# Performance work log

Hardware: AMD Instinct MI355X
Metric: run time of the kernel (lower is better)

Reference implementation:

```python
import jax, jax.numpy as jnp
import numpy as np

N_NODES = 50000


def setup_inputs() -> dict:
    key = jax.random.key(0)
    ks = jax.random.split(key, 10)
    B, N, D, H, O = 2, N_NODES, 128, 128, 10
    x = jax.random.normal(ks[0], (B, N, D), dtype=jnp.float32)
    edge_index = jax.random.randint(ks[1], (2, 800000), 0, N, dtype=jnp.int32)
    s = lambda fan_in: 1.0 / np.sqrt(fan_in)
    W  = jax.random.uniform(ks[2], (D, H), jnp.float32, -s(D), s(D))
    b  = jnp.zeros((H,), jnp.float32)
    W1 = jax.random.uniform(ks[3], (H, H // 2), jnp.float32, -s(H), s(H))
    b1 = jnp.zeros((H // 2,), jnp.float32)
    W2 = jax.random.uniform(ks[4], (H // 2, H // 4), jnp.float32, -s(H // 2), s(H // 2))
    b2 = jnp.zeros((H // 4,), jnp.float32)
    W3 = jax.random.uniform(ks[5], (H // 4, O), jnp.float32, -s(H // 4), s(H // 4))
    b3 = jnp.zeros((O,), jnp.float32)
    return {"x": x, "edge_index": edge_index, "W": W, "b": b,
            "W1": W1, "b1": b1, "W2": W2, "b2": b2, "W3": W3, "b3": b3}


def reference(x, edge_index, W, b, W1, b1, W2, b2, W3, b3):
    # GraphConvolution (Kipf): support = x @ W; out[dst] += support[src]; + b
    src, dst = edge_index[0], edge_index[1]
    support = jnp.einsum("bnd,dh->bnh", x, W)          # [B, N, H]
    msgs = support[:, src, :]                            # [B, E, H] gather
    agg = jnp.zeros_like(support).at[:, dst, :].add(msgs)  # scatter-add
    h = jax.nn.gelu(agg + b, approximate=False)          # GELU (torch default erf)
    # dropout is identity at inference (training=False)
    h = jax.nn.relu(jnp.einsum("bnh,hk->bnk", h, W1) + b1)
    h = jax.nn.relu(jnp.einsum("bnk,km->bnm", h, W2) + b2)
    h = jnp.einsum("bnm,mo->bno", h, W3) + b3            # [B, N, O]
    return h.mean(axis=1)                                # [B, O]
```

## Files before the change

### kernel.cpp

```cpp
#include <hip/hip_runtime.h>
#include <math.h>

#define NN 50000
#define DD 128
#define HH 128
#define L1 64
#define L2 32
#define OO 10

#define NW0 16384
#define NW1 8192
#define NW2 2048
#define NWT (NW0 + NW1 + NW2)

typedef short v8s __attribute__((ext_vector_type(8)));
typedef float v4f __attribute__((ext_vector_type(4)));

__device__ __forceinline__ float bf2f_lo(unsigned u) { return __uint_as_float(u << 16); }
__device__ __forceinline__ float bf2f_hi(unsigned u) { return __uint_as_float(u & 0xffff0000u); }
__device__ __forceinline__ unsigned short f2bf(float f) {
    unsigned u = __float_as_uint(f);
    return (unsigned short)((u + 0x7fffu + ((u >> 16) & 1u)) >> 16);
}
__device__ __forceinline__ unsigned pack2(float lo, float hi) {
    return (unsigned)f2bf(lo) | ((unsigned)f2bf(hi) << 16);
}
__device__ __forceinline__ float gelu_f(float v) {
    return 0.5f * v * (1.f + erff(v * 0.70710678118654752f));
}

__global__ __launch_bounds__(256) void k_prep(
    const float* __restrict__ x, unsigned short* __restrict__ xb,
    const int* __restrict__ ei, int* __restrict__ counts,
    const float* __restrict__ W, const float* __restrict__ W1,
    const float* __restrict__ W2, unsigned short* __restrict__ wtp,
    unsigned short* __restrict__ w1tp, unsigned short* __restrict__ w2tp,
    int* __restrict__ ssf, int nfill, unsigned* __restrict__ zrow, int E)
{
    const int gid = blockIdx.x * 256 + threadIdx.x;
    const int stride = gridDim.x * 256;

    for (int i = gid; i < NWT; i += stride) {
        if (i < NW0) {
            const int e = i & 7, ln = (i >> 3) & 63, ks = (i >> 9) & 3, ct = i >> 11;
            wtp[i] = f2bf(W[(ks * 32 + (ln >> 4) * 8 + e) * HH + ct * 16 + (ln & 15)]);
        } else if (i < NW0 + NW1) {
            const int j = i - NW0;
            const int e = j & 7, ln = (j >> 3) & 63, ks = (j >> 9) & 3, ct = j >> 11;
            w1tp[j] = f2bf(W1[(ks * 32 + (ln >> 4) * 8 + e) * L1 + ct * 16 + (ln & 15)]);
        } else {
            const int j = i - NW0 - NW1;
            const int e = j & 7, ln = (j >> 3) & 63, ks = (j >> 9) & 1, ct = j >> 10;
            w2tp[j] = f2bf(W2[(ks * 32 + (ln >> 4) * 8 + e) * L2 + ct * 16 + (ln & 15)]);
        }
    }
    if (zrow != nullptr && gid < 128) zrow[gid] = 0u;
    for (int i = gid; i < nfill; i += stride) ssf[i] = NN;
    const int HALF = NN * 32;
    for (int idx = gid; idx < 2 * HALF; idx += stride) {
        const int b = (idx >= HALF) ? 1 : 0;
        const int j = idx - b * HALF;
        const int n = j >> 5;
        const int c4 = j & 31;
        const float4 v = *(const float4*)(x + ((size_t)b * NN + n) * DD + c4 * 4);
        ushort4 o;
        o.x = f2bf(v.x); o.y = f2bf(v.y); o.z = f2bf(v.z); o.w = f2bf(v.w);
        *(ushort4*)(xb + ((size_t)n * 2 + b) * DD + c4 * 4) = o;
    }
    for (int e = gid; e < E; e += stride)
        atomicAdd(&counts[ei[(size_t)E + e]], 1);
}

__global__ __launch_bounds__(1024) void k_scan1(
    const int* __restrict__ counts, int* __restrict__ offsets,
    int* __restrict__ blksum, int n)
{
    __shared__ int wsum[16], woff[16];
    const int tid = threadIdx.x, lane = tid & 63, wv = tid >> 6;
    const int i = blockIdx.x * 1024 + tid;
    int v = (i < n) ? ((counts[i] + 7) & ~7) : 0;
    int x = v;
    #pragma unroll
    for (int d = 1; d < 64; d <<= 1) { int t = __shfl_up(x, d); if (lane >= d) x += t; }
    if (lane == 63) wsum[wv] = x;
    __syncthreads();
    if (wv == 0 && lane < 16) {
        int y = wsum[lane];
        #pragma unroll
        for (int d = 1; d < 16; d <<= 1) { int t = __shfl_up(y, d); if (lane >= d) y += t; }
        woff[lane] = y - wsum[lane];
        if (lane == 15) blksum[blockIdx.x] = y;
    }
    __syncthreads();
    if (i < n) offsets[i] = woff[wv] + (x - v);
}

__global__ __launch_bounds__(1024) void k_scan2(
    int* __restrict__ offsets, const int* __restrict__ blksum, int nblk, int n)
{
    __shared__ int base_sh, tot_sh;
    const int tid = threadIdx.x, lane = tid & 63, wv = tid >> 6;
    if (wv == 0) {
        int v = (lane < nblk) ? blksum[lane] : 0;
        int x = v;
        #pragma unroll
        for (int d = 1; d < 64; d <<= 1) { int t = __shfl_up(x, d); if (lane >= d) x += t; }
        int incl = __shfl(x, blockIdx.x);
        int own  = __shfl(v, blockIdx.x);
        int tot  = __shfl(x, nblk - 1);
        if (lane == 0) { base_sh = incl - own; tot_sh = tot; }
    }
    __syncthreads();
    const int i = blockIdx.x * 1024 + tid;
    if (i < n) offsets[i] += base_sh;
    if (blockIdx.x == nblk - 1 && tid == 0) offsets[n] = tot_sh;
}

__global__ __launch_bounds__(256) void k_bucket(
    const int* __restrict__ ei, const int* __restrict__ offsets,
    int* __restrict__ cursor, int* __restrict__ ss, int E)
{
    int e = blockIdx.x * 256 + threadIdx.x;
    if (e < E) {
        int d = ei[E + e];
        int pos = offsets[d] + atomicAdd(&cursor[d], 1);
        ss[pos] = ei[e];
    }
}

template<bool FUSED>
__global__ __launch_bounds__(256, 8) void k_mlp_t(
    const unsigned short* __restrict__ src,
    const int* __restrict__ offsets, const int* __restrict__ ss,
    const unsigned short* __restrict__ wtp, const float* __restrict__ b0v,
    const unsigned short* __restrict__ w1tp, const float* __restrict__ b1v,
    const unsigned short* __restrict__ w2tp, const float* __restrict__ b2v,
    float* __restrict__ partials, int srows)
{
    __shared__ __align__(16) unsigned char upool[32 * 136 * 2];
    __shared__ __align__(16) unsigned short h1b[32 * 72];
    __shared__ float b0s[DD], b1s[L1], b2s[L2];
    __shared__ float oacc[64];
    unsigned short* xa  = (unsigned short*)upool;
    unsigned short* hsb = (unsigned short*)upool;
    float* h2p = (float*)upool;

    const int tid = threadIdx.x;
    const int row0 = blockIdx.x * 32;
    const int lane = tid & 63;
    const int w = tid >> 6;

    if (tid < DD) b0s[tid] = b0v[tid];
    if (tid < L1) b1s[tid] = b1v[tid];
    if (tid < L2) b2s[tid] = b2v[tid];
    if (tid < 64) oacc[tid] = 0.f;

    if (FUSED) {
        const int half4 = (lane >> 5) * 4;
        const int co = (lane & 31) * 8;
        #pragma unroll
        for (int j = 0; j < 4; ++j) {
            const int ln = w * 4 + j;
            const int d = blockIdx.x * 16 + ln;
            int s0 = 0, s1 = 0;
            if (d < NN) { s0 = offsets[d]; s1 = offsets[d + 1]; }
            float a[8];
            #pragma unroll
            for (int t = 0; t < 8; ++t) a[t] = 0.f;
            uint4 nidx;
            if (s0 < s1) nidx = *(const uint4*)(ss + s0 + half4);
            for (int i = s0; i < s1; ) {
                const uint4 idx = nidx;
                const int inext = i + 8;
                if (inext < s1) nidx = *(const uint4*)(ss + inext + half4);
                const uint4 r0 = *(const uint4*)(src + (size_t)idx.x * 256 + co);
                const uint4 r1 = *(const uint4*)(src + (size_t)idx.y * 256 + co);
                const uint4 r2 = *(const uint4*)(src + (size_t)idx.z * 256 + co);
                const uint4 r3 = *(const uint4*)(src + (size_t)idx.w * 256 + co);
                a[0] += bf2f_lo(r0.x); a[1] += bf2f_hi(r0.x);
                a[2] += bf2f_lo(r0.y); a[3] += bf2f_hi(r0.y);
                a[4] += bf2f_lo(r0.z); a[5] += bf2f_hi(r0.z);
                a[6] += bf2f_lo(r0.w); a[7] += bf2f_hi(r0.w);
                a[0] += bf2f_lo(r1.x); a[1] += bf2f_hi(r1.x);
                a[2] += bf2f_lo(r1.y); a[3] += bf2f_hi(r1.y);
                a[4] += bf2f_lo(r1.z); a[5] += bf2f_hi(r1.z);
                a[6] += bf2f_lo(r1.w); a[7] += bf2f_hi(r1.w);
                a[0] += bf2f_lo(r2.x); a[1] += bf2f_hi(r2.x);
                a[2] += bf2f_lo(r2.y); a[3] += bf2f_hi(r2.y);
                a[4] += bf2f_lo(r2.z); a[5] += bf2f_hi(r2.z);
                a[6] += bf2f_lo(r2.w); a[7] += bf2f_hi(r2.w);
                a[0] += bf2f_lo(r3.x); a[1] += bf2f_hi(r3.x);
                a[2] += bf2f_lo(r3.y); a[3] += bf2f_hi(r3.y);
                a[4] += bf2f_lo(r3.z); a[5] += bf2f_hi(r3.z);
                a[6] += bf2f_lo(r3.w); a[7] += bf2f_hi(r3.w);
                i = inext;
            }
            #pragma unroll
            for (int t = 0; t < 8; ++t) a[t] += __shfl_xor(a[t], 32);
            if (lane < 32) {
                const int tr = ln * 2 + (lane >> 4);
                const int col = (lane & 15) * 8;
                uint4 o;
                o.x = pack2(a[0], a[1]); o.y = pack2(a[2], a[3]);
                o.z = pack2(a[4], a[5]); o.w = pack2(a[6], a[7]);
                *(uint4*)(&xa[tr * 136 + col]) = o;
            }
        }
    } else {
        for (int u = tid * 8; u < 32 * DD; u += 2048) {
            const int r = u >> 7, c = u & 127;
            uint4 raw = make_uint4(0, 0, 0, 0);
            if (row0 + r < srows) raw = *(const uint4*)(src + (size_t)(row0 + r) * HH + c);
            *(uint4*)(&xa[r * 136 + c]) = raw;
        }
    }
    __syncthreads();

    const int lm = lane & 15;
    const int q = lane >> 4;
    const int r1 = (w & 1) * 16;
    const int ch = w >> 1;

    {
        v4f acc[4];
        #pragma unroll
        for (int i = 0; i < 4; ++i) acc[i] = (v4f)(0.f);
        #pragma unroll
        for (int ks = 0; ks < 4; ++ks) {
            const int k0 = ks * 32 + q * 8;
            const v8s af = *(const v8s*)(&xa[(r1 + lm) * 136 + k0]);
            #pragma unroll
            for (int ct = 0; ct < 4; ++ct) {
                const int ctg = ch * 4 + ct;
                const v8s bf = *(const v8s*)(wtp + ((size_t)(ctg * 4 + ks) * 64 + lane) * 8);
                acc[ct] = __builtin_amdgcn_mfma_f32_16x16x32_bf16(af, bf, acc[ct], 0, 0, 0);
            }
        }
        __syncthreads();

        #pragma unroll
        for (int ct = 0; ct < 4; ++ct) {
            const int col = ch * 64 + ct * 16 + lm;
            const float bias = b0s[col];
            #pragma unroll
            for (int r = 0; r < 4; ++r)
                hsb[(r1 + q * 4 + r) * 136 + col] = f2bf(gelu_f(acc[ct][r] + bias));
        }
    }
    __syncthreads();

    {
        v4f a1[2];
        a1[0] = (v4f)(0.f); a1[1] = (v4f)(0.f);
        #pragma unroll
        for (int ks = 0; ks < 4; ++ks) {
            const int k0 = ks * 32 + q * 8;
            const v8s af = *(const v8s*)(&hsb[(r1 + lm) * 136 + k0]);
            #pragma unroll
            for (int ct = 0; ct < 2; ++ct) {
                const int ctg = ch * 2 + ct;
                const v8s bf = *(const v8s*)(w1tp + ((size_t)(ctg * 4 + ks) * 64 + lane) * 8);
                a1[ct] = __builtin_amdgcn_mfma_f32_16x16x32_bf16(af, bf, a1[ct], 0, 0, 0);
            }
        }
        #pragma unroll
        for (int ct = 0; ct < 2; ++ct) {
            const int col = ch * 32 + ct * 16 + lm;
            const float bias = b1s[col];
            #pragma unroll
            for (int r = 0; r < 4; ++r)
                h1b[(r1 + q * 4 + r) * 72 + col] = f2bf(fmaxf(a1[ct][r] + bias, 0.f));
        }
    }
    __syncthreads();

    {
        v4f a2 = (v4f)(0.f);
        #pragma unroll
        for (int ks = 0; ks < 2; ++ks) {
            const int k0 = ks * 32 + q * 8;
            const v8s af = *(const v8s*)(&h1b[(r1 + lm) * 72 + k0]);
            const v8s bf = *(const v8s*)(w2tp + ((size_t)(ch * 2 + ks) * 64 + lane) * 8);
            a2 = __builtin_amdgcn_mfma_f32_16x16x32_bf16(af, bf, a2, 0, 0, 0);
        }
        __syncthreads();
        const int col = ch * 16 + lm;
        const float bias = b2s[col];
        #pragma unroll
        for (int r = 0; r < 4; ++r)
            h2p[(r1 + q * 4 + r) * 36 + col] = fmaxf(a2[r] + bias, 0.f);
    }
    __syncthreads();

    {
        const int c = tid & 31;
        const int g = tid >> 5;
        float p0 = 0.f, p1 = 0.f;
        #pragma unroll
        for (int i = 0; i < 4; ++i) {
            const int r = g * 4 + i;
            if (row0 + r < srows) {
                const float v = h2p[r * 36 + c];
                if (r & 1) p1 += v; else p0 += v;
            }
        }
        if (p0 != 0.f) atomicAdd(&oacc[c], p0);
        if (p1 != 0.f) atomicAdd(&oacc[32 + c], p1);
    }
    __syncthreads();
    if (tid < 64) partials[(size_t)blockIdx.x * 64 + tid] = oacc[tid];
}

__global__ __launch_bounds__(256) void k_scatter(
    const int* __restrict__ ei, const unsigned short* __restrict__ xb,
    float* __restrict__ aggf, int E)
{
    const int tid = threadIdx.x;
    const int eg = tid >> 6;
    const int lane = tid & 63;
    const int e = blockIdx.x * 4 + eg;
    if (e >= E) return;
    const int src = ei[e];
    const int dst = ei[E + e];
    const uint2 r = *(const uint2*)(xb + (size_t)src * 256 + lane * 4);
    float* ap = aggf + (size_t)dst * 256 + lane * 4;
    unsafeAtomicAdd(ap + 0, bf2f_lo(r.x));
    unsafeAtomicAdd(ap + 1, bf2f_hi(r.x));
    unsafeAtomicAdd(ap + 2, bf2f_lo(r.y));
    unsafeAtomicAdd(ap + 3, bf2f_hi(r.y));
}

__global__ __launch_bounds__(256) void k_cvt(
    const float* __restrict__ in, unsigned short* __restrict__ outb, int n)
{
    int i = blockIdx.x * 256 + threadIdx.x;
    if (i < n) outb[i] = f2bf(in[i]);
}

__global__ __launch_bounds__(256) void k_reduce_final(
    const float* __restrict__ partials, float* __restrict__ accum, int nblk,
    int* __restrict__ dcnt, const float* __restrict__ W3,
    const float* __restrict__ b3v, float* __restrict__ out)
{
    __shared__ float lsum[4][64];
    __shared__ int lastf;
    const int t = threadIdx.x & 63;
    const int w = threadIdx.x >> 6;
    float s = 0.f;
    for (int g = blockIdx.x * 4 + w; g < nblk; g += gridDim.x * 4)
        s += partials[(size_t)g * 64 + t];
    lsum[w][t] = s;
    __syncthreads();
    if (threadIdx.x < 64) {
        const float v = lsum[0][t] + lsum[1][t] + lsum[2][t] + lsum[3][t];
        unsafeAtomicAdd(&accum[t], v);
    }
    __threadfence();
    __syncthreads();
    if (threadIdx.x == 0)
        lastf = (atomicAdd(dcnt, 1) == (int)gridDim.x - 1) ? 1 : 0;
    __syncthreads();
    if (lastf && threadIdx.x < 2 * OO) {
        const int b = threadIdx.x / OO, o = threadIdx.x % OO;
        float acc = b3v[o];
        const float inv = 1.0f / (float)NN;
        #pragma unroll
        for (int j = 0; j < L2; ++j)
            acc += (unsafeAtomicAdd(&accum[b * 32 + j], 0.f) * inv) * W3[j * OO + o];
        out[threadIdx.x] = acc;
    }
}

extern "C" void kernel_launch(void* const* d_in, const int* in_sizes, int n_in,
                              void* d_out, int out_size, void* d_ws, size_t ws_size,
                              hipStream_t stream) {
    const float* x  = (const float*)d_in[0];
    const int*   ei = (const int*)d_in[1];
    const float* W  = (const float*)d_in[2];
    const float* b0 = (const float*)d_in[3];
    const float* W1 = (const float*)d_in[4];
    const float* b1 = (const float*)d_in[5];
    const float* W2 = (const float*)d_in[6];
    const float* b2 = (const float*)d_in[7];
    const float* W3 = (const float*)d_in[8];
    const float* b3 = (const float*)d_in[9];
    float* out = (float*)d_out;

    const int E = in_sizes[1] / 2;
    const int rows = 2 * NN;
    const int nblk = (rows + 31) / 32;
    const int nsb = (NN + 1023) / 1024;
    const int SSN = E + 7 * NN + 8;

    unsigned short* xb = (unsigned short*)d_ws;
    unsigned* zrow     = (unsigned*)(xb + (size_t)rows * HH);
    int*   ss       = (int*)(zrow + 128);
    float* partials = (float*)(ss + SSN);
    float* accum    = partials + (size_t)nblk * 64;
    int*   dcnt     = (int*)(accum + 64);
    int*   counts   = dcnt + 16;
    int*   cursor   = counts + NN;
    int*   offsets  = cursor + NN;
    int*   blksum   = offsets + NN + 1;
    unsigned short* wtp = (unsigned short*)(((uintptr_t)(blksum + 64) + 15) & ~(uintptr_t)15);
    unsigned short* w1tp = wtp + NW0;
    unsigned short* w2tp = w1tp + NW1;
    const size_t need_csr = (size_t)((unsigned short*)(w2tp + NW2) - (unsigned short*)d_ws)
                            * sizeof(unsigned short) + 16;

    unsigned short* f_aggb = xb + (size_t)rows * HH;
    float* f_partials = (float*)(f_aggb + (size_t)rows * HH);
    float* f_accum    = f_partials + (size_t)nblk * 64;
    int*   f_dcnt     = (int*)(f_accum + 64);
    unsigned short* f_wtp = (unsigned short*)(((uintptr_t)(f_dcnt + 16) + 15) & ~(uintptr_t)15);
    unsigned short* f_w1tp = f_wtp + NW0;
    unsigned short* f_w2tp = f_w1tp + NW1;
    float* f_aggf     = (float*)(((uintptr_t)(f_w2tp + NW2) + 15) & ~(uintptr_t)15);
    const size_t need_fb = (size_t)((char*)(f_aggf + (size_t)rows * HH) - (char*)d_ws) + 16;

    if (ws_size >= need_csr && nsb <= 64) {
        hipMemsetAsync(accum, 0, (80 + 2 * (size_t)NN) * sizeof(int), stream);
        k_prep<<<dim3(2048), dim3(256), 0, stream>>>(
            x, xb, ei, counts, W, W1, W2, wtp, w1tp, w2tp, ss, SSN, zrow, E);
        k_scan1<<<dim3(nsb), dim3(1024), 0, stream>>>(counts, offsets, blksum, NN);
        k_scan2<<<dim3(nsb), dim3(1024), 0, stream>>>(offsets, blksum, nsb, NN);
        k_bucket<<<dim3((E + 255) / 256), dim3(256), 0, stream>>>(ei, offsets, cursor, ss, E);
        k_mlp_t<true><<<dim3(nblk), dim3(256), 0, stream>>>(
            xb, offsets, ss, wtp, b0, w1tp, b1, w2tp, b2, partials, rows);
        k_reduce_final<<<dim3(64), dim3(256), 0, stream>>>(
            partials, accum, nblk, dcnt, W3, b3, out);
    } else if (ws_size >= need_fb) {
        hipMemsetAsync(f_accum, 0, 80 * sizeof(int), stream);
        hipMemsetAsync(f_aggf, 0, (size_t)rows * HH * sizeof(float), stream);
        k_prep<<<dim3(2048), dim3(256), 0, stream>>>(
            x, xb, ei, (int*)f_dcnt , W, W1, W2, f_wtp, f_w1tp, f_w2tp,
            (int*)f_dcnt, 0, nullptr, 0);
        k_scatter<<<dim3((E + 3) / 4), dim3(256), 0, stream>>>(ei, xb, f_aggf, E);
        k_cvt<<<dim3((rows * HH + 255) / 256), dim3(256), 0, stream>>>(f_aggf, f_aggb, rows * HH);
        k_mlp_t<false><<<dim3(nblk), dim3(256), 0, stream>>>(
            f_aggb, nullptr, nullptr, f_wtp, b0, f_w1tp, b1, f_w2tp, b2, f_partials, rows);
        k_reduce_final<<<dim3(64), dim3(256), 0, stream>>>(
            f_partials, f_accum, nblk, f_dcnt, W3, b3, out);
    }
}
```

Before: 277.6 us.

## Fuse scan passes and final reduction via last-block atomics to cut launches

Merges the two-kernel prefix scan into one kernel. The last block to finish, detected with an atomic counter, scans the block sums into per-block offsets that consumers add on the fly. It also folds the final reduction and W3 projection into the tail of the MLP kernel using the same last-block pattern, removing two kernel launches. The cost is a serial reduction over all partials by a single block and extra offset lookups in the bucket and gather code.

```diff
diff --git a/kernel.cpp b/kernel.cpp
--- a/kernel.cpp
+++ b/kernel.cpp
@@ -39,7 +39,6 @@
 {
     const int gid = blockIdx.x * 256 + threadIdx.x;
     const int stride = gridDim.x * 256;
-
     for (int i = gid; i < NWT; i += stride) {
         if (i < NW0) {
             const int e = i & 7, ln = (i >> 3) & 63, ks = (i >> 9) & 3, ct = i >> 11;
@@ -71,11 +70,13 @@
         atomicAdd(&counts[ei[(size_t)E + e]], 1);
 }
 
-__global__ __launch_bounds__(1024) void k_scan1(
+__global__ __launch_bounds__(1024) void k_scanA(
     const int* __restrict__ counts, int* __restrict__ offsets,
-    int* __restrict__ blksum, int n)
+    int* __restrict__ blksum, int* __restrict__ blkoff,
+    int* __restrict__ wtotb, int* __restrict__ scnt, int n, int nblk)
 {
     __shared__ int wsum[16], woff[16];
+    __shared__ int lastf;
     const int tid = threadIdx.x, lane = tid & 63, wv = tid >> 6;
     const int i = blockIdx.x * 1024 + tid;
     int v = (i < n) ? ((counts[i] + 7) & ~7) : 0;
@@ -93,37 +94,31 @@
     }
     __syncthreads();
     if (i < n) offsets[i] = woff[wv] + (x - v);
-}
-
-__global__ __launch_bounds__(1024) void k_scan2(
-    int* __restrict__ offsets, const int* __restrict__ blksum, int nblk, int n)
-{
-    __shared__ int base_sh, tot_sh;
-    const int tid = threadIdx.x, lane = tid & 63, wv = tid >> 6;
-    if (wv == 0) {
-        int v = (lane < nblk) ? blksum[lane] : 0;
-        int x = v;
-        #pragma unroll
-        for (int d = 1; d < 64; d <<= 1) { int t = __shfl_up(x, d); if (lane >= d) x += t; }
-        int incl = __shfl(x, blockIdx.x);
-        int own  = __shfl(v, blockIdx.x);
-        int tot  = __shfl(x, nblk - 1);
-        if (lane == 0) { base_sh = incl - own; tot_sh = tot; }
-    }
-    __syncthreads();
-    const int i = blockIdx.x * 1024 + tid;
-    if (i < n) offsets[i] += base_sh;
-    if (blockIdx.x == nblk - 1 && tid == 0) offsets[n] = tot_sh;
+
+    __threadfence();
+    __syncthreads();
+    if (tid == 0)
+        lastf = (atomicAdd(scnt, 1) == nblk - 1) ? 1 : 0;
+    __syncthreads();
+    if (lastf && wv == 0) {
+        int s = (lane < nblk) ? atomicAdd(&blksum[lane], 0) : 0;
+        int xx = s;
+        #pragma unroll
+        for (int d = 1; d < 64; d <<= 1) { int t = __shfl_up(xx, d); if (lane >= d) xx += t; }
+        if (lane < nblk) blkoff[lane] = xx - s;
+        if (lane == nblk - 1) wtotb[0] = xx;
+    }
 }
 
 __global__ __launch_bounds__(256) void k_bucket(
     const int* __restrict__ ei, const int* __restrict__ offsets,
-    int* __restrict__ cursor, int* __restrict__ ss, int E)
+    const int* __restrict__ blkoff, int* __restrict__ cursor,
+    int* __restrict__ ss, int E)
 {
     int e = blockIdx.x * 256 + threadIdx.x;
     if (e < E) {
         int d = ei[E + e];
-        int pos = offsets[d] + atomicAdd(&cursor[d], 1);
+        int pos = offsets[d] + blkoff[d >> 10] + atomicAdd(&cursor[d], 1);
         ss[pos] = ei[e];
     }
 }
@@ -132,15 +127,20 @@
 __global__ __launch_bounds__(256, 8) void k_mlp_t(
     const unsigned short* __restrict__ src,
     const int* __restrict__ offsets, const int* __restrict__ ss,
+    const int* __restrict__ blkoff, const int* __restrict__ wtotb,
     const unsigned short* __restrict__ wtp, const float* __restrict__ b0v,
     const unsigned short* __restrict__ w1tp, const float* __restrict__ b1v,
     const unsigned short* __restrict__ w2tp, const float* __restrict__ b2v,
-    float* __restrict__ partials, int srows)
+    float* __restrict__ partials, int srows,
+    int* __restrict__ dcnt, const float* __restrict__ W3,
+    const float* __restrict__ b3v, float* __restrict__ out)
 {
     __shared__ __align__(16) unsigned char upool[32 * 136 * 2];
     __shared__ __align__(16) unsigned short h1b[32 * 72];
     __shared__ float b0s[DD], b1s[L1], b2s[L2];
     __shared__ float oacc[64];
+    __shared__ float lsum[4][64];
+    __shared__ int lastf;
     unsigned short* xa  = (unsigned short*)upool;
     unsigned short* hsb = (unsigned short*)upool;
     float* h2p = (float*)upool;
@@ -158,12 +158,16 @@
     if (FUSED) {
         const int half4 = (lane >> 5) * 4;
         const int co = (lane & 31) * 8;
+        const int wtot = wtotb[0];
         #pragma unroll
         for (int j = 0; j < 4; ++j) {
             const int ln = w * 4 + j;
             const int d = blockIdx.x * 16 + ln;
             int s0 = 0, s1 = 0;
-            if (d < NN) { s0 = offsets[d]; s1 = offsets[d + 1]; }
+            if (d < NN) {
+                s0 = offsets[d] + blkoff[d >> 10];
+                s1 = (d + 1 < NN) ? offsets[d + 1] + blkoff[(d + 1) >> 10] : wtot;
+            }
             float a[8];
             #pragma unroll
             for (int t = 0; t < 8; ++t) a[t] = 0.f;
@@ -237,7 +241,6 @@
             }
         }
         __syncthreads();
-
         #pragma unroll
         for (int ct = 0; ct < 4; ++ct) {
             const int col = ch * 64 + ct * 16 + lm;
@@ -309,6 +312,33 @@
     }
     __syncthreads();
     if (tid < 64) partials[(size_t)blockIdx.x * 64 + tid] = oacc[tid];
+
+    __threadfence();
+    __syncthreads();
+    if (tid == 0)
+        lastf = (atomicAdd(dcnt, 1) == (int)gridDim.x - 1) ? 1 : 0;
+    __syncthreads();
+    if (lastf) {
+        const int t = tid & 63;
+        const int NTb = (int)gridDim.x;
+        float s = 0.f;
+        for (int g = w; g < NTb; g += 4)
+            s += unsafeAtomicAdd(&partials[(size_t)g * 64 + t], 0.f);
+        lsum[w][t] = s;
+        __syncthreads();
+        if (tid < 64)
+            oacc[t] = lsum[0][t] + lsum[1][t] + lsum[2][t] + lsum[3][t];
+        __syncthreads();
+        if (tid < 2 * OO) {
+            const int b = tid / OO, o = tid % OO;
+            float acc = b3v[o];
+            const float inv = 1.0f / (float)NN;
+            #pragma unroll
+            for (int j = 0; j < L2; ++j)
+                acc += (oacc[b * 32 + j] * inv) * W3[j * OO + o];
+            out[tid] = acc;
+        }
+    }
 }
 
 __global__ __launch_bounds__(256) void k_scatter(
@@ -335,40 +365,6 @@
 {
     int i = blockIdx.x * 256 + threadIdx.x;
     if (i < n) outb[i] = f2bf(in[i]);
-}
-
-__global__ __launch_bounds__(256) void k_reduce_final(
-    const float* __restrict__ partials, float* __restrict__ accum, int nblk,
-    int* __restrict__ dcnt, const float* __restrict__ W3,
-    const float* __restrict__ b3v, float* __restrict__ out)
-{
-    __shared__ float lsum[4][64];
-    __shared__ int lastf;
-    const int t = threadIdx.x & 63;
-    const int w = threadIdx.x >> 6;
-    float s = 0.f;
-    for (int g = blockIdx.x * 4 + w; g < nblk; g += gridDim.x * 4)
-        s += partials[(size_t)g * 64 + t];
-    lsum[w][t] = s;
-    __syncthreads();
-    if (threadIdx.x < 64) {
-        const float v = lsum[0][t] + lsum[1][t] + lsum[2][t] + lsum[3][t];
-        unsafeAtomicAdd(&accum[t], v);
-    }
-    __threadfence();
-    __syncthreads();
-    if (threadIdx.x == 0)
-        lastf = (atomicAdd(dcnt, 1) == (int)gridDim.x - 1) ? 1 : 0;
-    __syncthreads();
-    if (lastf && threadIdx.x < 2 * OO) {
-        const int b = threadIdx.x / OO, o = threadIdx.x % OO;
-        float acc = b3v[o];
-        const float inv = 1.0f / (float)NN;
-        #pragma unroll
-        for (int j = 0; j < L2; ++j)
-            acc += (unsafeAtomicAdd(&accum[b * 32 + j], 0.f) * inv) * W3[j * OO + o];
-        out[threadIdx.x] = acc;
-    }
 }
 
 extern "C" void kernel_launch(void* const* d_in, const int* in_sizes, int n_in,
@@ -388,58 +384,58 @@
 
     const int E = in_sizes[1] / 2;
     const int rows = 2 * NN;
-    const int nblk = (rows + 31) / 32;
-    const int nsb = (NN + 1023) / 1024;
+    const int NT = (rows + 31) / 32;
+    const int nsc = (NN + 1023) / 1024;
     const int SSN = E + 7 * NN + 8;
 
     unsigned short* xb = (unsigned short*)d_ws;
     unsigned* zrow     = (unsigned*)(xb + (size_t)rows * HH);
     int*   ss       = (int*)(zrow + 128);
     float* partials = (float*)(ss + SSN);
-    float* accum    = partials + (size_t)nblk * 64;
-    int*   dcnt     = (int*)(accum + 64);
-    int*   counts   = dcnt + 16;
+    int*   dcnt     = (int*)(partials + (size_t)NT * 64);
+    int*   scnt     = dcnt + 16;
+    int*   counts   = scnt + 16;
     int*   cursor   = counts + NN;
     int*   offsets  = cursor + NN;
     int*   blksum   = offsets + NN + 1;
-    unsigned short* wtp = (unsigned short*)(((uintptr_t)(blksum + 64) + 15) & ~(uintptr_t)15);
+    int*   blkoff   = blksum + 64;
+    int*   wtotb    = blkoff + 64;
+    unsigned short* wtp = (unsigned short*)(((uintptr_t)(wtotb + 16) + 15) & ~(uintptr_t)15);
     unsigned short* w1tp = wtp + NW0;
     unsigned short* w2tp = w1tp + NW1;
-    const size_t need_csr = (size_t)((unsigned short*)(w2tp + NW2) - (unsigned short*)d_ws)
-                            * sizeof(unsigned short) + 16;
-
-    unsigned short* f_aggb = xb + (size_t)rows * HH;
-    float* f_partials = (float*)(f_aggb + (size_t)rows * HH);
-    float* f_accum    = f_partials + (size_t)nblk * 64;
-    int*   f_dcnt     = (int*)(f_accum + 64);
-    unsigned short* f_wtp = (unsigned short*)(((uintptr_t)(f_dcnt + 16) + 15) & ~(uintptr_t)15);
-    unsigned short* f_w1tp = f_wtp + NW0;
-    unsigned short* f_w2tp = f_w1tp + NW1;
-    float* f_aggf     = (float*)(((uintptr_t)(f_w2tp + NW2) + 15) & ~(uintptr_t)15);
-    const size_t need_fb = (size_t)((char*)(f_aggf + (size_t)rows * HH) - (char*)d_ws) + 16;
-
-    if (ws_size >= need_csr && nsb <= 64) {
-        hipMemsetAsync(accum, 0, (80 + 2 * (size_t)NN) * sizeof(int), stream);
+    const size_t need_csr = (size_t)((char*)(w2tp + NW2) - (char*)d_ws) + 16;
+    const size_t zeroN = 32 + 2 * (size_t)NN;
+
+    unsigned short* g_aggb = xb + (size_t)rows * HH;
+    float* g_partials = (float*)(g_aggb + (size_t)rows * HH);
+    int*   g_dcnt     = (int*)(g_partials + (size_t)NT * 64);
+    unsigned short* g_wtp = (unsigned short*)(((uintptr_t)(g_dcnt + 16) + 15) & ~(uintptr_t)15);
+    unsigned short* g_w1tp = g_wtp + NW0;
+    unsigned short* g_w2tp = g_w1tp + NW1;
+    float* g_aggf     = (float*)(((uintptr_t)(g_w2tp + NW2) + 15) & ~(uintptr_t)15);
+    const size_t need_fb = (size_t)((char*)(g_aggf + (size_t)rows * HH) - (char*)d_ws) + 16;
+
+    if (ws_size >= need_csr && nsc <= 49) {
+        hipMemsetAsync(dcnt, 0, zeroN * sizeof(int), stream);
         k_prep<<<dim3(2048), dim3(256), 0, stream>>>(
             x, xb, ei, counts, W, W1, W2, wtp, w1tp, w2tp, ss, SSN, zrow, E);
-        k_scan1<<<dim3(nsb), dim3(1024), 0, stream>>>(counts, offsets, blksum, NN);
-        k_scan2<<<dim3(nsb), dim3(1024), 0, stream>>>(offsets, blksum, nsb, NN);
-        k_bucket<<<dim3((E + 255) / 256), dim3(256), 0, stream>>>(ei, offsets, cursor, ss, E);
-        k_mlp_t<true><<<dim3(nblk), dim3(256), 0, stream>>>(
-            xb, offsets, ss, wtp, b0, w1tp, b1, w2tp, b2, partials, rows);
-        k_reduce_final<<<dim3(64), dim3(256), 0, stream>>>(
-            partials, accum, nblk, dcnt, W3, b3, out);
+        k_scanA<<<dim3(nsc), dim3(1024), 0, stream>>>(
+            counts, offsets, blksum, blkoff, wtotb, scnt, NN, nsc);
+        k_bucket<<<dim3((E + 255) / 256), dim3(256), 0, stream>>>(
+            ei, offsets, blkoff, cursor, ss, E);
+        k_mlp_t<true><<<dim3(NT), dim3(256), 0, stream>>>(
+            xb, offsets, ss, blkoff, wtotb, wtp, b0, w1tp, b1, w2tp, b2,
+            partials, rows, dcnt, W3, b3, out);
     } else if (ws_size >= need_fb) {
-        hipMemsetAsync(f_accum, 0, 80 * sizeof(int), stream);
-        hipMemsetAsync(f_aggf, 0, (size_t)rows * HH * sizeof(float), stream);
+        hipMemsetAsync(g_dcnt, 0, 16 * sizeof(int), stream);
+        hipMemsetAsync(g_aggf, 0, (size_t)rows * HH * sizeof(float), stream);
         k_prep<<<dim3(2048), dim3(256), 0, stream>>>(
-            x, xb, ei, (int*)f_dcnt , W, W1, W2, f_wtp, f_w1tp, f_w2tp,
-            (int*)f_dcnt, 0, nullptr, 0);
-        k_scatter<<<dim3((E + 3) / 4), dim3(256), 0, stream>>>(ei, xb, f_aggf, E);
-        k_cvt<<<dim3((rows * HH + 255) / 256), dim3(256), 0, stream>>>(f_aggf, f_aggb, rows * HH);
-        k_mlp_t<false><<<dim3(nblk), dim3(256), 0, stream>>>(
-            f_aggb, nullptr, nullptr, f_wtp, b0, f_w1tp, b1, f_w2tp, b2, f_partials, rows);
-        k_reduce_final<<<dim3(64), dim3(256), 0, stream>>>(
-            f_partials, f_accum, nblk, f_dcnt, W3, b3, out);
-    }
-}
+            x, xb, ei, g_dcnt , W, W1, W2, g_wtp, g_w1tp, g_w2tp,
+            g_dcnt, 0, nullptr, 0);
+        k_scatter<<<dim3((E + 3) / 4), dim3(256), 0, stream>>>(ei, xb, g_aggf, E);
+        k_cvt<<<dim3((rows * HH + 255) / 256), dim3(256), 0, stream>>>(g_aggf, g_aggb, rows * HH);
+        k_mlp_t<false><<<dim3(NT), dim3(256), 0, stream>>>(
+            g_aggb, nullptr, nullptr, nullptr, nullptr, g_wtp, b0, g_w1tp, b1,
+            g_w2tp, b2, g_partials, rows, g_dcnt, W3, b3, out);
+    }
+}
```

After: 706.2 us. +154.4%, slower.
